# Kernel tuning notes

Measured on AMD Instinct MI355X. Metric: run time of the kernel, lower is better.

Reference implementation:

```python
import jax, jax.numpy as jnp
import numpy as np

N_HEAD = 16
POSE = 5
YAW = 1
END_X, END_Y = 18, 32
THETA = 1000.0
LN_EPS = 1e-5

def compute_axial_cis(dim, end_x, end_y, theta):
    # Axial 2D rotary: dim is per-head dim; dim//4 freqs per spatial axis.
    n = dim // 4
    freqs = 1.0 / (theta ** (jnp.arange(0, dim, 4)[:n].astype(jnp.float32) / dim))
    t = jnp.arange(end_x * end_y, dtype=jnp.float32)
    t_x = t % end_x
    t_y = jnp.floor(t / end_x)
    ang = jnp.concatenate([t_x[:, None] * freqs[None, :], t_y[:, None] * freqs[None, :]], axis=-1)  # [L, dim//2]
    return jnp.cos(ang), jnp.sin(ang)

def apply_rotary(x, cos, sin):
    # x: [B,H,L,D]; complex pairing = consecutive (even, odd) lanes, as in view_as_complex
    xe, xo = x[..., 0::2], x[..., 1::2]
    oe = xe * cos - xo * sin
    oo = xe * sin + xo * cos
    return jnp.stack([oe, oo], axis=-1).reshape(x.shape)

def layernorm(z, g, b):
    m = jnp.mean(z, axis=-1, keepdims=True)
    v = jnp.mean(jnp.square(z - m), axis=-1, keepdims=True)
    return (z - m) * jax.lax.rsqrt(v + LN_EPS) * g + b

def setup_inputs() -> dict:
    key = jax.random.key(0)
    ks = jax.random.split(key, 8)
    B, T, C = 16, 582, 1024
    x = jax.random.normal(ks[0], (B, T, C), dtype=jnp.float32)
    # additive causal mask (0 keep / -1e9 masked), as a float attn_mask
    causal = jnp.tril(jnp.ones((T, T), dtype=jnp.float32))
    attn_mask = jnp.broadcast_to(jnp.where(causal > 0, 0.0, -1e9), (B, T, T))
    s = 0.02
    Wq = jax.random.normal(ks[1], (C, C), dtype=jnp.float32) * s
    Wk = jax.random.normal(ks[2], (C, C), dtype=jnp.float32) * s
    Wv = jax.random.normal(ks[3], (C, C), dtype=jnp.float32) * s
    Wo = jax.random.normal(ks[4], (C, C), dtype=jnp.float32) * s
    q_ln_g = jnp.ones((C,), jnp.float32); q_ln_b = jnp.zeros((C,), jnp.float32)
    k_ln_g = jnp.ones((C,), jnp.float32); k_ln_b = jnp.zeros((C,), jnp.float32)
    return {"x": x, "attn_mask": attn_mask, "Wq": Wq, "Wk": Wk, "Wv": Wv, "Wo": Wo,
            "q_ln_g": q_ln_g, "q_ln_b": q_ln_b, "k_ln_g": k_ln_g, "k_ln_b": k_ln_b}

def reference(x, attn_mask, Wq, Wk, Wv, Wo, q_ln_g, q_ln_b, k_ln_g, k_ln_b):
    B, T, C = x.shape
    H = N_HEAD
    D = C // H
    q = layernorm(x @ Wq.T, q_ln_g, q_ln_b)
    k = layernorm(x @ Wk.T, k_ln_g, k_ln_b)
    v = (x @ Wv.T).reshape(B, T, H, D).transpose(0, 2, 1, 3)
    q = q.reshape(B, T, H, D).transpose(0, 2, 1, 3)
    k = k.reshape(B, T, H, D).transpose(0, 2, 1, 3)
    prefix = POSE + YAW
    if T > prefix:  # static shape condition
        cos, sin = compute_axial_cis(D, END_X, END_Y, THETA)
        L = T - prefix
        cos, sin = cos[:L], sin[:L]  # [L, D//2]
        q = jnp.concatenate([q[:, :, :prefix], apply_rotary(q[:, :, prefix:], cos, sin)], axis=2)
        k = jnp.concatenate([k[:, :, :prefix], apply_rotary(k[:, :, prefix:], cos, sin)], axis=2)
    scale = 1.0 / jnp.sqrt(jnp.float32(D))
    scores = jnp.einsum("bhqd,bhkd->bhqk", q, k) * scale + attn_mask[:, None, :, :]
    att = jax.nn.softmax(scores, axis=-1)
    y = jnp.einsum("bhqk,bhkd->bhqd", att, v)
    y = y.transpose(0, 2, 1, 3).reshape(B, T, C)
    return y @ Wo.T
```

## Files before the change

### kernel.cpp

```cpp
#include <hip/hip_runtime.h>
#include <hip/hip_bf16.h>

typedef short bf16x8 __attribute__((ext_vector_type(8)));
typedef short bf16x4 __attribute__((ext_vector_type(4)));
typedef float f32x4  __attribute__((ext_vector_type(4)));

#define LDP 72

__device__ __forceinline__ float bits2f(short u) {
  return __uint_as_float(((unsigned int)(unsigned short)u) << 16);
}
__device__ __forceinline__ short f2bits(float f) {
  __hip_bfloat16 h = __float2bfloat16(f);
  return *reinterpret_cast<short*>(&h);
}
__device__ __forceinline__ void gld16(const short* g, short* l) {
  __builtin_amdgcn_global_load_lds(
      (const __attribute__((address_space(1))) void*)g,
      (__attribute__((address_space(3))) void*)l, 16, 0, 0);
}

__global__ __launch_bounds__(256)
void cvt_x_kernel(const float* __restrict__ src, short* __restrict__ dst, long n) {
  long i = ((long)blockIdx.x * 256 + threadIdx.x) * 4;
  if (i + 3 < n) {
    float4 v = *(const float4*)(src + i);
    bf16x4 o;
    o[0] = f2bits(v.x); o[1] = f2bits(v.y); o[2] = f2bits(v.z); o[3] = f2bits(v.w);
    *(bf16x4*)(dst + i) = o;
  }
}

__global__ __launch_bounds__(256)
void cvt_w_kernel(const float* __restrict__ w0, const float* __restrict__ w1,
                  const float* __restrict__ w2, const float* __restrict__ w3,
                  short* __restrict__ dst) {
  long i = ((long)blockIdx.x * 256 + threadIdx.x) * 4;
  int sel = (int)(i >> 20);
  const float* s = (sel == 0) ? w0 : (sel == 1) ? w1 : (sel == 2) ? w2 : w3;
  long off = i & ((1L << 20) - 1);
  float4 v = *(const float4*)(s + off);
  bf16x4 o;
  o[0] = f2bits(v.x); o[1] = f2bits(v.y); o[2] = f2bits(v.z); o[3] = f2bits(v.w);
  *(bf16x4*)(dst + i) = o;
}

template<int MODE>
__global__ __launch_bounds__(256)
void gemm_nt(const short* __restrict__ A, const short* __restrict__ Bm,
             float* __restrict__ OutF, short* __restrict__ Oq,
             short* __restrict__ Ok, short* __restrict__ Ov,
             int M, int K, int N, int T, int TPAD) {
  __shared__ short As[128 * 64];
  __shared__ short Bs[128 * 64];
  const int tid = threadIdx.x;
  const int w = tid >> 6, l = tid & 63;
  const int wr = w >> 1, wc = w & 1;
  const int lg = l >> 4, lo = l & 15;

  const int R = gridDim.x, C2 = gridDim.y;
  const int d = blockIdx.y * R + blockIdx.x;
  int r, c;
  if ((R & 7) == 1 && (C2 & 7) == 0) {
    const int x = d & 7, i = d >> 3;
    const int C8 = C2 >> 3;
    const int chunk = R * C8;
    const int b9 = R >> 3;
    const int rows0 = b9 + 1;
    if (x == 0) { c = i / rows0; r = i % rows0; }
    else {
      const int nb = b9 * C2;
      if (i < nb) { c = i / b9; r = rows0 + (x - 1) * b9 + i % b9; }
      else { int p = chunk + (x - 1) * C8 + (i - nb); c = p / rows0; r = p % rows0; }
    }
  } else { r = blockIdx.x; c = blockIdx.y; }
  const long row0 = (long)r * 128;
  const long col0 = (long)c * 128;

  const short* pa[4]; const short* pb[4]; short* la[4]; short* lb[4];
#pragma unroll
  for (int j = 0; j < 4; ++j) {
    const int ch = w * 4 + j;
    const int off = ch * 1024 + l * 16;
    const int row = off >> 7;
    const int lc  = (off & 127) ^ ((row & 7) << 4);
    long ga = row0 + row; if (ga > M - 1) ga = M - 1;
    pa[j] = &A[ga * K + (lc >> 1)];
    pb[j] = &Bm[(col0 + row) * K + (lc >> 1)];
    la[j] = &As[ch * 512];
    lb[j] = &Bs[ch * 512];
  }

  f32x4 acc[4][4] = {};

  for (int kt = 0; kt < K; kt += 64) {
    __syncthreads();
#pragma unroll
    for (int j = 0; j < 4; ++j) {
      gld16(pa[j] + kt, la[j]);
      gld16(pb[j] + kt, lb[j]);
    }
    __syncthreads();
    bf16x8 af[4][2], bfr[4][2];
#pragma unroll
    for (int mi = 0; mi < 4; ++mi)
#pragma unroll
      for (int ks = 0; ks < 2; ++ks) {
        int pe = (ks * 32 + lg * 8) ^ ((lo & 7) << 3);
        af[mi][ks] = *(const bf16x8*)(&As[(wr * 64 + mi * 16 + lo) * 64 + pe]);
      }
#pragma unroll
    for (int ni = 0; ni < 4; ++ni)
#pragma unroll
      for (int ks = 0; ks < 2; ++ks) {
        int pe = (ks * 32 + lg * 8) ^ ((lo & 7) << 3);
        bfr[ni][ks] = *(const bf16x8*)(&Bs[(wc * 64 + ni * 16 + lo) * 64 + pe]);
      }
#pragma unroll
    for (int mi = 0; mi < 4; ++mi)
#pragma unroll
      for (int ni = 0; ni < 4; ++ni)
#pragma unroll
        for (int ks = 0; ks < 2; ++ks)
          acc[mi][ni] = __builtin_amdgcn_mfma_f32_16x16x32_bf16(af[mi][ks], bfr[ni][ks], acc[mi][ni], 0, 0, 0);
  }

#pragma unroll
  for (int mi = 0; mi < 4; ++mi) {
#pragma unroll
    for (int rr = 0; rr < 4; ++rr) {
      long m = row0 + wr * 64 + mi * 16 + lg * 4 + rr;
      if (m >= M) continue;
#pragma unroll
      for (int ni = 0; ni < 4; ++ni) {
        long n = col0 + wc * 64 + ni * 16 + lo;
        float v = acc[mi][ni][rr];
        if constexpr (MODE == 2) {
          OutF[m * (long)N + n] = v;
        } else {
          if (n < 1024) {
            Oq[m * 1024 + n] = f2bits(v);
          } else if (n < 2048) {
            Ok[m * 1024 + (n - 1024)] = f2bits(v);
          } else {
            long b = m / T, t = m - b * T;
            long nn = n - 2048, h = nn >> 6, dd = nn & 63;
            Ov[((b * 16 + h) * 64 + dd) * TPAD + t] = f2bits(v);
          }
        }
      }
    }
  }
}

__global__ __launch_bounds__(256)
void ln_rope_kernel(const short* __restrict__ qpre, const short* __restrict__ kpre,
                    const float* __restrict__ qg, const float* __restrict__ qb2,
                    const float* __restrict__ kg, const float* __restrict__ kb2,
                    short* __restrict__ qa, short* __restrict__ ka, int T) {
  const int row = blockIdx.x;
  const short* in; const float *g, *be; short* out;
  if (blockIdx.y == 0) { in = qpre; g = qg; be = qb2; out = qa; }
  else                 { in = kpre; g = kg; be = kb2; out = ka; }
  const int tid = threadIdx.x;
  const int c0 = tid * 4;

  bf16x4 xv = *(const bf16x4*)(&in[(long)row * 1024 + c0]);
  float xf[4];
  float s = 0.f, sq = 0.f;
#pragma unroll
  for (int i = 0; i < 4; ++i) { xf[i] = bits2f(xv[i]); s += xf[i]; sq += xf[i] * xf[i]; }
#pragma unroll
  for (int o = 1; o < 64; o <<= 1) { s += __shfl_xor(s, o); sq += __shfl_xor(sq, o); }
  __shared__ float red[8];
  const int w = tid >> 6, l = tid & 63;
  if (l == 0) { red[w] = s; red[4 + w] = sq; }
  __syncthreads();
  s  = red[0] + red[1] + red[2] + red[3];
  sq = red[4] + red[5] + red[6] + red[7];
  const float mean = s * (1.0f / 1024.0f);
  const float var  = sq * (1.0f / 1024.0f) - mean * mean;
  const float rstd = rsqrtf(var + 1e-5f);

  float4 gv = *(const float4*)(&g[c0]);
  float4 bv = *(const float4*)(&be[c0]);
  float z[4];
  z[0] = (xf[0] - mean) * rstd * gv.x + bv.x;
  z[1] = (xf[1] - mean) * rstd * gv.y + bv.y;
  z[2] = (xf[2] - mean) * rstd * gv.z + bv.z;
  z[3] = (xf[3] - mean) * rstd * gv.w + bv.w;

  const int t = row % T;
  const int p = t - 6;
  if (p >= 0) {
    const float tx = (float)(p % 18);
    const float ty = (float)(p / 18);
    const int jbase = (c0 & 63) >> 1;
#pragma unroll
    for (int q2 = 0; q2 < 2; ++q2) {
      const int jj = jbase + q2;
      const int i  = jj & 15;
      const float freq = exp2f(-(float)i * 0.6228615177913804f);
      const float ang  = ((jj < 16) ? tx : ty) * freq;
      float sv, cv;
      sincosf(ang, &sv, &cv);
      const float xe = z[q2 * 2], xo = z[q2 * 2 + 1];
      z[q2 * 2]     = xe * cv - xo * sv;
      z[q2 * 2 + 1] = xe * sv + xo * cv;
    }
  }
  const long b = row / T;
  const int h = c0 >> 6, d = c0 & 63;
  bf16x4 ov;
#pragma unroll
  for (int i = 0; i < 4; ++i) ov[i] = f2bits(z[i]);
  *(bf16x4*)(&out[(((b * 16 + h) * T) + t) * 64 + d]) = ov;
}

__global__ __launch_bounds__(256)
void attn_kernel(const short* __restrict__ Q, const short* __restrict__ Kk,
                 const short* __restrict__ Vt, short* __restrict__ Y,
                 int T, int TPAD) {
  __shared__ short Ps[4][16 * LDP];
  const int tid = threadIdx.x;
  const int w = tid >> 6, l = tid & 63, lg = l >> 4, lo = l & 15;
  const int qb = gridDim.x - 1 - blockIdx.x;
  const int bh = blockIdx.y;
  const int b = bh >> 4, h = bh & 15;
  const long qbase = (long)bh * T * 64;
  const long vbase = (long)bh * 64;
  short* Pw = &Ps[w][0];

  const long qrow_l = qb * 64 + w * 16 + lo;
  bf16x8 qf[2];
  qf[0] = *(const bf16x8*)(&Q[qbase + qrow_l * 64 + lg * 8]);
  qf[1] = *(const bf16x8*)(&Q[qbase + qrow_l * 64 + 32 + lg * 8]);

  float mrow[4], lsum[4];
  f32x4 oacc[4] = {};
#pragma unroll
  for (int r = 0; r < 4; ++r) { mrow[r] = -3e38f; lsum[r] = 0.f; }
  const float SCL = 0.125f * 1.44269504f;
  const int nkt = qb + 1;

  for (int kt = 0; kt < nkt; ++kt) {
    bf16x8 kfr[4][2], vf[4][2];
#pragma unroll
    for (int ni = 0; ni < 4; ++ni)
#pragma unroll
      for (int kk = 0; kk < 2; ++kk)
        kfr[ni][kk] = *(const bf16x8*)(&Kk[qbase + (long)(kt * 64 + ni * 16 + lo) * 64 + kk * 32 + lg * 8]);
#pragma unroll
    for (int ni = 0; ni < 4; ++ni)
#pragma unroll
      for (int kk = 0; kk < 2; ++kk)
        vf[ni][kk] = *(const bf16x8*)(&Vt[(vbase + ni * 16 + lo) * TPAD + kt * 64 + kk * 32 + lg * 8]);

    f32x4 sf[4] = {};
#pragma unroll
    for (int ni = 0; ni < 4; ++ni)
#pragma unroll
      for (int kk = 0; kk < 2; ++kk)
        sf[ni] = __builtin_amdgcn_mfma_f32_16x16x32_bf16(qf[kk], kfr[ni][kk], sf[ni], 0, 0, 0);

    float pm[4][4], tmax[4];
#pragma unroll
    for (int r = 0; r < 4; ++r) tmax[r] = -3e38f;
#pragma unroll
    for (int ni = 0; ni < 4; ++ni)
#pragma unroll
      for (int r = 0; r < 4; ++r) {
        int key  = kt * 64 + ni * 16 + lo;
        int qrow = qb * 64 + w * 16 + lg * 4 + r;
        float sv = sf[ni][r] * SCL;
        if (key > qrow || key >= T) sv = -3e38f;
        pm[ni][r] = sv;
        tmax[r] = fmaxf(tmax[r], sv);
      }
#pragma unroll
    for (int r = 0; r < 4; ++r)
#pragma unroll
      for (int o = 1; o < 16; o <<= 1) tmax[r] = fmaxf(tmax[r], __shfl_xor(tmax[r], o));

    bool need = !__all(tmax[0] <= mrow[0] && tmax[1] <= mrow[1] &&
                       tmax[2] <= mrow[2] && tmax[3] <= mrow[3]);
    if (need) {
#pragma unroll
      for (int r = 0; r < 4; ++r) {
        float mn = fmaxf(mrow[r], tmax[r]);
        float fsc = exp2f(mrow[r] - mn);
        mrow[r] = mn;
        lsum[r] *= fsc;
#pragma unroll
        for (int ni = 0; ni < 4; ++ni) oacc[ni][r] *= fsc;
      }
    }
    float psum[4] = {0.f, 0.f, 0.f, 0.f};
#pragma unroll
    for (int ni = 0; ni < 4; ++ni)
#pragma unroll
      for (int r = 0; r < 4; ++r) {
        float pv = exp2f(pm[ni][r] - mrow[r]);
        pm[ni][r] = pv;
        psum[r] += pv;
      }
#pragma unroll
    for (int r = 0; r < 4; ++r) {
#pragma unroll
      for (int o = 1; o < 16; o <<= 1) psum[r] += __shfl_xor(psum[r], o);
      lsum[r] += psum[r];
    }

#pragma unroll
    for (int ni = 0; ni < 4; ++ni)
#pragma unroll
      for (int r = 0; r < 4; ++r)
        Pw[(lg * 4 + r) * LDP + ni * 16 + lo] = f2bits(pm[ni][r]);

#pragma unroll
    for (int kk = 0; kk < 2; ++kk) {
      bf16x8 pf = *(const bf16x8*)(&Pw[lo * LDP + kk * 32 + lg * 8]);
#pragma unroll
      for (int ni = 0; ni < 4; ++ni)
        oacc[ni] = __builtin_amdgcn_mfma_f32_16x16x32_bf16(pf, vf[ni][kk], oacc[ni], 0, 0, 0);
    }
  }

#pragma unroll
  for (int r = 0; r < 4; ++r) {
    int tq = qb * 64 + w * 16 + lg * 4 + r;
    if (tq >= T) continue;
    float inv = 1.0f / lsum[r];
#pragma unroll
    for (int ni = 0; ni < 4; ++ni) {
      float o = oacc[ni][r] * inv;
      Y[((long)b * T + tq) * 1024 + h * 64 + ni * 16 + lo] = f2bits(o);
    }
  }
}

extern "C" void kernel_launch(void* const* d_in, const int* in_sizes, int n_in,
                              void* d_out, int out_size, void* d_ws, size_t ws_size,
                              hipStream_t stream) {
  const float* x   = (const float*)d_in[0];
  const float* Wq  = (const float*)d_in[2];
  const float* Wk  = (const float*)d_in[3];
  const float* Wv  = (const float*)d_in[4];
  const float* Wo  = (const float*)d_in[5];
  const float* qg  = (const float*)d_in[6];
  const float* qb2 = (const float*)d_in[7];
  const float* kg  = (const float*)d_in[8];
  const float* kb2 = (const float*)d_in[9];

  const int B = 16, T = 582, C = 1024;
  const int M = B * T;
  const int TPAD = 584;

  short* ws = (short*)d_ws;
  const long E  = (long)M * C;
  const long EV = (long)B * 16 * 64 * TPAD;
  short* xb   = ws;
  short* qpre = ws + E;
  short* kpre = ws + 2 * E;
  short* ka   = ws + 3 * E;
  short* vat  = ws + 4 * E;
  short* wb   = ws + 4 * E + EV + 1024;
  short* qa   = xb;
  short* y    = qpre;
  float* out  = (float*)d_out;
  (void)ws_size; (void)in_sizes; (void)n_in; (void)out_size;

  const long WE = 1L << 20;

  cvt_x_kernel<<<(int)(E / 4 / 256), 256, 0, stream>>>(x, xb, E);
  cvt_w_kernel<<<(int)(4 * WE / 4 / 256), 256, 0, stream>>>(Wq, Wk, Wv, Wo, wb);

  dim3 gqkv((M + 127) / 128, 3072 / 128);
  gemm_nt<3><<<gqkv, 256, 0, stream>>>(xb, wb, nullptr, qpre, kpre, vat, M, C, 3072, T, TPAD);
  ln_rope_kernel<<<dim3(M, 2), 256, 0, stream>>>(qpre, kpre, qg, qb2, kg, kb2, qa, ka, T);
  attn_kernel<<<dim3((T + 63) / 64, B * 16), 256, 0, stream>>>(qa, ka, vat, y, T, TPAD);
  dim3 gout((M + 127) / 128, C / 128);
  gemm_nt<2><<<gout, 256, 0, stream>>>(y, wb + 3 * WE, out, nullptr, nullptr, nullptr, M, C, C, T, TPAD);
}
```

Before: 293.2 us.

## Double-buffer K/V tiles in LDS for attention and drop GEMM tile swizzle

The attention kernel now stages each 64-key K and V tile into double-buffered shared memory with async global-to-LDS loads, prefetching the next tile while computing the current one. Fragments are read from swizzled LDS instead of straight from global memory, and s_setprio is raised around the MFMA sections. Separately, the GEMM drops its custom XCD-aware block remapping and uses plain blockIdx ordering. This adds a __syncthreads per key tile and more LDS use, which may lower occupancy, and removing the remap could hurt cache locality across XCDs.

Result: faster. 264.6 us (-9.8%).

```diff
diff --git a/kernel.cpp b/kernel.cpp
--- a/kernel.cpp
+++ b/kernel.cpp
@@ -57,25 +57,8 @@
   const int w = tid >> 6, l = tid & 63;
   const int wr = w >> 1, wc = w & 1;
   const int lg = l >> 4, lo = l & 15;
-
-  const int R = gridDim.x, C2 = gridDim.y;
-  const int d = blockIdx.y * R + blockIdx.x;
-  int r, c;
-  if ((R & 7) == 1 && (C2 & 7) == 0) {
-    const int x = d & 7, i = d >> 3;
-    const int C8 = C2 >> 3;
-    const int chunk = R * C8;
-    const int b9 = R >> 3;
-    const int rows0 = b9 + 1;
-    if (x == 0) { c = i / rows0; r = i % rows0; }
-    else {
-      const int nb = b9 * C2;
-      if (i < nb) { c = i / b9; r = rows0 + (x - 1) * b9 + i % b9; }
-      else { int p = chunk + (x - 1) * C8 + (i - nb); c = p / rows0; r = p % rows0; }
-    }
-  } else { r = blockIdx.x; c = blockIdx.y; }
-  const long row0 = (long)r * 128;
-  const long col0 = (long)c * 128;
+  const long row0 = (long)blockIdx.x * 128;
+  const long col0 = (long)blockIdx.y * 128;
 
   const short* pa[4]; const short* pb[4]; short* la[4]; short* lb[4];
 #pragma unroll
@@ -128,13 +111,13 @@
 #pragma unroll
   for (int mi = 0; mi < 4; ++mi) {
 #pragma unroll
-    for (int rr = 0; rr < 4; ++rr) {
-      long m = row0 + wr * 64 + mi * 16 + lg * 4 + rr;
+    for (int r = 0; r < 4; ++r) {
+      long m = row0 + wr * 64 + mi * 16 + lg * 4 + r;
       if (m >= M) continue;
 #pragma unroll
       for (int ni = 0; ni < 4; ++ni) {
         long n = col0 + wc * 64 + ni * 16 + lo;
-        float v = acc[mi][ni][rr];
+        float v = acc[mi][ni][r];
         if constexpr (MODE == 2) {
           OutF[m * (long)N + n] = v;
         } else {
@@ -221,6 +204,8 @@
 void attn_kernel(const short* __restrict__ Q, const short* __restrict__ Kk,
                  const short* __restrict__ Vt, short* __restrict__ Y,
                  int T, int TPAD) {
+  __shared__ short Ks[2][64 * 64];
+  __shared__ short Vs[2][64 * 64];
   __shared__ short Ps[4][16 * LDP];
   const int tid = threadIdx.x;
   const int w = tid >> 6, l = tid & 63, lg = l >> 4, lo = l & 15;
@@ -231,6 +216,23 @@
   const long vbase = (long)bh * 64;
   short* Pw = &Ps[w][0];
 
+  int srow[2], scolb[2];
+#pragma unroll
+  for (int p = 0; p < 2; ++p) {
+    int off = p * 4096 + tid * 16;
+    srow[p] = off >> 7;
+    scolb[p] = (off & 127) ^ ((srow[p] & 7) << 4);
+  }
+  auto STAGE = [&](int kt, int buf) {
+#pragma unroll
+    for (int p = 0; p < 2; ++p) {
+      short* kd = &Ks[buf][(p * 4096 + w * 1024) >> 1];
+      short* vd = &Vs[buf][(p * 4096 + w * 1024) >> 1];
+      gld16(&Kk[qbase + (long)(kt * 64 + srow[p]) * 64 + (scolb[p] >> 1)], kd);
+      gld16(&Vt[(vbase + srow[p]) * TPAD + (long)kt * 64 + (scolb[p] >> 1)], vd);
+    }
+  };
+
   const long qrow_l = qb * 64 + w * 16 + lo;
   bf16x8 qf[2];
   qf[0] = *(const bf16x8*)(&Q[qbase + qrow_l * 64 + lg * 8]);
@@ -243,25 +245,23 @@
   const float SCL = 0.125f * 1.44269504f;
   const int nkt = qb + 1;
 
+  STAGE(0, 0);
   for (int kt = 0; kt < nkt; ++kt) {
-    bf16x8 kfr[4][2], vf[4][2];
-#pragma unroll
-    for (int ni = 0; ni < 4; ++ni)
-#pragma unroll
-      for (int kk = 0; kk < 2; ++kk)
-        kfr[ni][kk] = *(const bf16x8*)(&Kk[qbase + (long)(kt * 64 + ni * 16 + lo) * 64 + kk * 32 + lg * 8]);
-#pragma unroll
-    for (int ni = 0; ni < 4; ++ni)
-#pragma unroll
-      for (int kk = 0; kk < 2; ++kk)
-        vf[ni][kk] = *(const bf16x8*)(&Vt[(vbase + ni * 16 + lo) * TPAD + kt * 64 + kk * 32 + lg * 8]);
+    const int cur = kt & 1;
+    __syncthreads();
+    if (kt + 1 < nkt) STAGE(kt + 1, cur ^ 1);
 
     f32x4 sf[4] = {};
-#pragma unroll
-    for (int ni = 0; ni < 4; ++ni)
-#pragma unroll
-      for (int kk = 0; kk < 2; ++kk)
-        sf[ni] = __builtin_amdgcn_mfma_f32_16x16x32_bf16(qf[kk], kfr[ni][kk], sf[ni], 0, 0, 0);
+    __builtin_amdgcn_s_setprio(1);
+#pragma unroll
+    for (int ni = 0; ni < 4; ++ni)
+#pragma unroll
+      for (int kk = 0; kk < 2; ++kk) {
+        int pe = (kk * 32 + lg * 8) ^ ((lo & 7) << 3);
+        bf16x8 kfr = *(const bf16x8*)(&Ks[cur][(ni * 16 + lo) * 64 + pe]);
+        sf[ni] = __builtin_amdgcn_mfma_f32_16x16x32_bf16(qf[kk], kfr, sf[ni], 0, 0, 0);
+      }
+    __builtin_amdgcn_s_setprio(0);
 
     float pm[4][4], tmax[4];
 #pragma unroll
@@ -317,13 +317,18 @@
       for (int r = 0; r < 4; ++r)
         Pw[(lg * 4 + r) * LDP + ni * 16 + lo] = f2bits(pm[ni][r]);
 
+    __builtin_amdgcn_s_setprio(1);
 #pragma unroll
     for (int kk = 0; kk < 2; ++kk) {
       bf16x8 pf = *(const bf16x8*)(&Pw[lo * LDP + kk * 32 + lg * 8]);
 #pragma unroll
-      for (int ni = 0; ni < 4; ++ni)
-        oacc[ni] = __builtin_amdgcn_mfma_f32_16x16x32_bf16(pf, vf[ni][kk], oacc[ni], 0, 0, 0);
-    }
+      for (int ni = 0; ni < 4; ++ni) {
+        int pe = (kk * 32 + lg * 8) ^ ((lo & 7) << 3);
+        bf16x8 vf = *(const bf16x8*)(&Vs[cur][(ni * 16 + lo) * 64 + pe]);
+        oacc[ni] = __builtin_amdgcn_mfma_f32_16x16x32_bf16(pf, vf, oacc[ni], 0, 0, 0);
+      }
+    }
+    __builtin_amdgcn_s_setprio(0);
   }
 
 #pragma unroll
```
